# Kernel tuning notes

Hardware: AMD Instinct MI355X
Metric: run time of the kernel (lower is better)

Reference implementation:

```python
import jax, jax.numpy as jnp
import numpy as np

B, T, N, D = 4, 128, 512, 32
CHEB_K, EMB, HEADS, TA_LAYERS, GCN_NUM, TCN_BLOCKS, KSIZE = 3, 10, 2, 2, 3, 3, 3


def setup_inputs() -> dict:
    key = jax.random.key(0)
    ks = jax.random.split(key, 12)
    x = jax.random.normal(ks[0], (B, T, N, D), jnp.float32)
    init_state = jnp.zeros((1, B, N, D), jnp.float32)  # unused by forward, kept for signature fidelity
    node_embeddings = jax.random.normal(ks[1], (N, EMB), jnp.float32)
    a = jax.random.uniform(ks[2], (N, N), jnp.float32)
    a = 0.5 * (a + a.T)
    adj = a / jnp.sum(a, axis=1, keepdims=True)  # row-normalized dense adjacency
    s = 0.05
    gcn_w = jax.random.normal(ks[3], (GCN_NUM, EMB, CHEB_K, D, D), jnp.float32) * s
    gcn_b = jax.random.normal(ks[4], (GCN_NUM, EMB, D), jnp.float32) * s
    tcn_w1 = jax.random.normal(ks[5], (TCN_BLOCKS, D, D, KSIZE), jnp.float32) * s
    tcn_b1 = jnp.zeros((TCN_BLOCKS, D), jnp.float32)
    tcn_w2 = jax.random.normal(ks[6], (TCN_BLOCKS, D, D, KSIZE), jnp.float32) * s
    tcn_b2 = jnp.zeros((TCN_BLOCKS, D), jnp.float32)
    ta_wq = jax.random.normal(ks[7], (TA_LAYERS, D, D), jnp.float32) * s
    ta_wk = jax.random.normal(ks[8], (TA_LAYERS, D, D), jnp.float32) * s
    ta_wv = jax.random.normal(ks[9], (TA_LAYERS, D, D), jnp.float32) * s
    ta_wo = jax.random.normal(ks[10], (TA_LAYERS, D, D), jnp.float32) * s
    ta_g = jnp.ones((TA_LAYERS, D), jnp.float32)
    ta_b = jnp.zeros((TA_LAYERS, D), jnp.float32)
    return dict(x=x, init_state=init_state, node_embeddings=node_embeddings, adj=adj,
                gcn_w=gcn_w, gcn_b=gcn_b, tcn_w1=tcn_w1, tcn_b1=tcn_b1, tcn_w2=tcn_w2,
                tcn_b2=tcn_b2, ta_wq=ta_wq, ta_wk=ta_wk, ta_wv=ta_wv, ta_wo=ta_wo,
                ta_g=ta_g, ta_b=ta_b)


def _cheb_supports(adj, k):
    I = jnp.eye(adj.shape[0], dtype=adj.dtype)
    s = [I, adj]
    for _ in range(2, k):
        s.append(2.0 * (adj @ s[-1]) - s[-2])
    return jnp.stack(s[:k])  # (k, N, N)


def _emb_gcn(h, supports, E, wp, bp):
    # h: (B,T,N,C); supports: (k,N,N); E: (N,EMB); wp: (EMB,k,C,O); bp: (EMB,O)
    xg = jnp.einsum('knm,btmc->btknc', supports, h)
    W = jnp.einsum('ne,ekco->nkco', E, wp)       # per-node Chebyshev weights
    bias = E @ bp                                 # (N,O)
    return jnp.einsum('btknc,nkco->btno', xg, W) + bias


def _causal_conv(y, w, b, dil):
    # y: (BN, C, T); w: (O, C, K)
    pad = (w.shape[-1] - 1) * dil
    out = jax.lax.conv_general_dilated(y, w, (1,), [(pad, 0)], rhs_dilation=(dil,),
                                       dimension_numbers=('NCH', 'OIH', 'NCH'))
    return out + b[None, :, None]


def _temporal_block(y, w1, b1, w2, b2, dil):
    o = jax.nn.relu(_causal_conv(y, w1, b1, dil))
    o = jax.nn.relu(_causal_conv(o, w2, b2, dil))
    return jax.nn.relu(o + y)  # residual (in_ch == out_ch)


def _layernorm(h, g, b):
    mu = jnp.mean(h, -1, keepdims=True)
    var = jnp.var(h, -1, keepdims=True)
    return (h - mu) * jax.lax.rsqrt(var + 1e-5) * g + b


def _attn_layer(h, wq, wk, wv, wo, g, b):
    # h: (BN, T, D) temporal self-attention
    bn, t, d = h.shape
    dh = d // HEADS
    scale = 1.0 / float(np.sqrt(dh))
    q = (h @ wq).reshape(bn, t, HEADS, dh)
    k = (h @ wk).reshape(bn, t, HEADS, dh)
    v = (h @ wv).reshape(bn, t, HEADS, dh)
    a = jax.nn.softmax(jnp.einsum('bqhd,bkhd->bhqk', q, k) * scale, axis=-1)
    o = jnp.einsum('bhqk,bkhd->bqhd', a, v).reshape(bn, t, d) @ wo
    return _layernorm(h + o, g, b)


def reference(x, init_state, node_embeddings, adj, gcn_w, gcn_b, tcn_w1, tcn_b1,
              tcn_w2, tcn_b2, ta_wq, ta_wk, ta_wv, ta_wo, ta_g, ta_b):
    supports = _cheb_supports(adj, CHEB_K)
    h = x
    for i in range(GCN_NUM):  # 3 stacked EmbGCN layers, vectorized over time
        h = _emb_gcn(h, supports, node_embeddings, gcn_w[i], gcn_b[i])
    b, t, n, d = h.shape
    y = jnp.transpose(h, (0, 2, 3, 1)).reshape(b * n, d, t)  # (BN, D, T)
    for i in range(TCN_BLOCKS):  # dilations 1,2,4
        y = _temporal_block(y, tcn_w1[i], tcn_b1[i], tcn_w2[i], tcn_b2[i], 2 ** i)
    h2 = jnp.transpose(y.reshape(b, n, d, t), (0, 1, 3, 2)).reshape(b * n, t, d)
    for i in range(TA_LAYERS):
        h2 = _attn_layer(h2, ta_wq[i], ta_wk[i], ta_wv[i], ta_wo[i], ta_g[i], ta_b[i])
    return jnp.transpose(h2.reshape(b, n, t, d), (0, 2, 1, 3))  # (B,T,N,D)
```

## Files before the change

### kernel.cpp

```cpp
#include <hip/hip_runtime.h>
#include <hip/hip_bf16.h>


typedef __attribute__((ext_vector_type(8))) short short8;
typedef __attribute__((ext_vector_type(4))) short short4v;
typedef __attribute__((ext_vector_type(4))) float float4v;

#define MFMA32(a, b, c) __builtin_amdgcn_mfma_f32_16x16x32_bf16((a), (b), (c), 0, 0, 0)
#if defined(__has_builtin)
#if __has_builtin(__builtin_amdgcn_mfma_f32_16x16x16_bf16)
#define MFMA16A(a, b, c) __builtin_amdgcn_mfma_f32_16x16x16_bf16((a), (b), (c), 0, 0, 0)
#endif
#endif
#ifndef MFMA16A
#define MFMA16A(a, b, c) __builtin_amdgcn_mfma_f32_16x16x16bf16_1k((a), (b), (c), 0, 0, 0)
#endif

#if defined(__has_builtin)
#if __has_builtin(__builtin_amdgcn_exp2f)
#define EXP2F(x) __builtin_amdgcn_exp2f(x)
#endif
#endif
#ifndef EXP2F
#define EXP2F(x) exp2f(x)
#endif

typedef const __attribute__((address_space(1))) unsigned int* gas_ptr;
typedef __attribute__((address_space(3))) unsigned int* las_ptr;
__device__ __forceinline__ void glds16(const void* g, void* l) {
  __builtin_amdgcn_global_load_lds((gas_ptr)g, (las_ptr)l, 16, 0, 0);
}

__device__ __forceinline__ unsigned int f2b2(float lo, float hi) {
  union { __hip_bfloat162 h; unsigned int u; } cv;
  cv.h = __float22bfloat162_rn(make_float2(lo, hi));
  return cv.u;
}
__device__ __forceinline__ unsigned short f2b(float f) {
  return (unsigned short)f2b2(f, f);
}
__device__ __forceinline__ float b2f(unsigned short u) {
  return __uint_as_float(((unsigned int)u) << 16);
}
__device__ __forceinline__ ushort4 f2b4(float a, float b, float c, float d) {
  union { unsigned int u[2]; ushort4 s; } cv;
  cv.u[0] = f2b2(a, b);
  cv.u[1] = f2b2(c, d);
  return cv.s;
}

__global__ void __launch_bounds__(256) prep_all(
    const float* __restrict__ adj, unsigned short* __restrict__ Sb,
    const float* __restrict__ emb, const float* __restrict__ gw,
    const float* __restrict__ gb, unsigned short* __restrict__ W8,
    float* __restrict__ biasn,
    const float* __restrict__ w1g, const float* __restrict__ w2g,
    unsigned short* __restrict__ Wt,
    const float* __restrict__ wqg, const float* __restrict__ wkg,
    const float* __restrict__ wvg, const float* __restrict__ wog,
    unsigned short* __restrict__ Wf,
    const float* __restrict__ x, unsigned short* __restrict__ H8,
    unsigned short* __restrict__ Hrm) {
  __shared__ unsigned short Asq[128 * 40];
  __shared__ unsigned short Bsq[128 * 40];
  int bid = blockIdx.x, tid = threadIdx.x;

  if (bid < 64) {
    int base = bid * 4096;
#pragma unroll
    for (int it = 0; it < 4; ++it) {
      int e = base + it * 1024 + tid * 4;
      float4 v = *(const float4*)&adj[e];
      union { unsigned int u[2]; ushort4 s; } pk;
      pk.u[0] = f2b2(v.x, v.y);
      pk.u[1] = f2b2(v.z, v.w);
      *(ushort4*)&Sb[e] = pk.s;
    }
    return;
  }
  if (bid < 80) {
    int tb = bid - 64;
    int mt = tb >> 2, jt = tb & 3;
    int m0 = mt * 128, j0 = jt * 128;
    int wave = tid >> 6, lane = tid & 63;
    int wm = wave >> 1, wj = wave & 1;
    int l15 = lane & 15, quad = lane >> 4;
    float4v acc[4][4];
#pragma unroll
    for (int a = 0; a < 4; ++a)
#pragma unroll
      for (int b = 0; b < 4; ++b) acc[a][b] = (float4v)0.f;
    for (int kt = 0; kt < 512; kt += 32) {
#pragma unroll
      for (int p = 0; p < 16; ++p) {
        int idx = p * 256 + tid;
        int m = idx >> 5, k = idx & 31;
        Asq[m * 40 + k] = f2b(adj[(m0 + m) * 512 + kt + k]);
      }
#pragma unroll
      for (int p = 0; p < 16; ++p) {
        int idx = p * 256 + tid;
        int k = idx >> 7, j = idx & 127;
        Bsq[j * 40 + k] = f2b(adj[(kt + k) * 512 + j0 + j]);
      }
      __syncthreads();
      short8 af[4], bfr[4];
#pragma unroll
      for (int mi = 0; mi < 4; ++mi)
        af[mi] = *(const short8*)&Asq[(wm * 64 + mi * 16 + l15) * 40 + quad * 8];
#pragma unroll
      for (int ji = 0; ji < 4; ++ji)
        bfr[ji] = *(const short8*)&Bsq[(wj * 64 + ji * 16 + l15) * 40 + quad * 8];
#pragma unroll
      for (int mi = 0; mi < 4; ++mi)
#pragma unroll
        for (int ji = 0; ji < 4; ++ji)
          acc[mi][ji] = MFMA32(af[mi], bfr[ji], acc[mi][ji]);
      __syncthreads();
    }
#pragma unroll
    for (int mi = 0; mi < 4; ++mi)
#pragma unroll
      for (int ji = 0; ji < 4; ++ji) {
        int j = j0 + wj * 64 + ji * 16 + l15;
#pragma unroll
        for (int r = 0; r < 4; ++r) {
          int m = m0 + wm * 64 + mi * 16 + quad * 4 + r;
          Sb[(512 + m) * 512 + j] =
              f2b(2.f * acc[mi][ji][r] - (m == j ? 1.f : 0.f));
        }
      }
    return;
  }
  if (bid < 1616) {
    int b2 = bid - 80;
    int i = b2 >> 9, n = b2 & 511;
    float ev[10];
#pragma unroll
    for (int e = 0; e < 10; ++e) ev[e] = emb[n * 10 + e];
    for (int idx = tid; idx < 3072; idx += 256) {
      int s = idx >> 10, c = (idx >> 5) & 31, o = idx & 31;
      float acc = 0.f;
#pragma unroll
      for (int e = 0; e < 10; ++e) acc += ev[e] * gw[(i * 10 + e) * 3072 + idx];
      W8[((i * 512 + n) * 3 + s) * 1024 + (c >> 3) * 256 + o * 8 + (c & 7)] =
          f2b(acc);
    }
    if (tid < 32) {
      float acc = 0.f;
#pragma unroll
      for (int e = 0; e < 10; ++e) acc += ev[e] * gb[(i * 10 + e) * 32 + tid];
      biasn[(i * 512 + n) * 32 + tid] = acc;
    }
    return;
  }
  if (bid < 1622) {
    int b2 = bid - 1616;
    int blk = b2 >> 1, conv = b2 & 1;
    const float* w = (conv ? w2g : w1g) + blk * 3072;
    for (int idx = tid; idx < 3072; idx += 256) {
      int kk = idx >> 10, rem = idx & 1023;
      int o = rem >> 5, c = rem & 31;
      Wt[b2 * 3072 + idx] = f2b(w[o * 96 + c * 3 + kk]);
    }
    return;
  }
  if (bid < 1654) {
    int idx = (bid - 1622) * 256 + tid;
    int L = idx >> 12;
    int mat = (idx >> 10) & 3;
    int nt = (idx >> 9) & 1;
    int lane = (idx >> 3) & 63;
    int j = idx & 7;
    int quad = lane >> 4, l15 = lane & 15;
    const float* base =
        (mat == 0 ? wqg : mat == 1 ? wkg : mat == 2 ? wvg : wog) + L * 1024;
    float v = base[(quad * 8 + j) * 32 + nt * 16 + l15];
    if (mat == 0) v *= 0.36067376022224085f;
    Wf[idx] = f2b(v);
    return;
  }
  {
    int b2 = bid - 1654;
    int nblk = b2 >> 3, part = b2 & 7;
    for (int qq = tid; qq < 2048; qq += 256) {
      int q = part * 2048 + qq;
      int bt = q >> 5, c = q & 31;
      const float* xb = x + bt * 16384 + nblk * 256 + c;
      float f[8];
#pragma unroll
      for (int s = 0; s < 8; ++s) f[s] = xb[s * 32];
      union { unsigned int u[4]; uint4 v; } pk;
      pk.u[0] = f2b2(f[0], f[1]);
      pk.u[1] = f2b2(f[2], f[3]);
      pk.u[2] = f2b2(f[4], f[5]);
      pk.u[3] = f2b2(f[6], f[7]);
      *(uint4*)&H8[nblk * 131072 + q * 8] = pk.v;
    }
    for (int qq = tid; qq < 2048; qq += 256) {
      int q = part * 2048 + qq;
      int s = q >> 11, e0 = (q & 2047) * 8;
      int bt = e0 >> 5, c0 = e0 & 31;
      const float* xb = x + bt * 16384 + (nblk * 8 + s) * 32 + c0;
      float4 v0 = *(const float4*)&xb[0];
      float4 v1 = *(const float4*)&xb[4];
      union { unsigned int u[4]; uint4 v; } pk;
      pk.u[0] = f2b2(v0.x, v0.y);
      pk.u[1] = f2b2(v0.z, v0.w);
      pk.u[2] = f2b2(v1.x, v1.y);
      pk.u[3] = f2b2(v1.z, v1.w);
      *(uint4*)&Hrm[(nblk * 8 + s) * 16384 + e0] = pk.v;
    }
  }
}

__global__ void __launch_bounds__(512) gcn_phaseA(
    const unsigned short* __restrict__ Sb,
    const unsigned short* __restrict__ H8,
    unsigned short* __restrict__ G) {
  __shared__ unsigned short As[2][256 * 32];
  __shared__ unsigned short Bs[2][4096];
  int bid0 = blockIdx.x;
  int nb = (bid0 & 7) * 64 + (bid0 >> 3);
  int mt = nb & 3, jt = nb >> 2;
  int m0 = mt * 256, j0 = jt * 128;
  int tid = threadIdx.x;
  int wave = tid >> 6, lane = tid & 63;
  int wm = wave >> 1, wj = wave & 1;
  int l15 = lane & 15, quad = lane >> 4;
  float4v acc[4][4];
#pragma unroll
  for (int a = 0; a < 4; ++a)
#pragma unroll
    for (int b = 0; b < 4; ++b) acc[a][b] = (float4v)0.f;

  int qa0 = tid, qa1 = tid + 512;
  int ma0 = qa0 >> 2, ca0 = ((qa0 & 3) ^ ((qa0 >> 3) & 3)) * 8;
  int ma1 = qa1 >> 2, ca1 = ((qa1 & 3) ^ ((qa1 >> 3) & 3)) * 8;
  const unsigned short* sb0 = &Sb[(m0 + ma0) * 512 + ca0];
  const unsigned short* sb1 = &Sb[(m0 + ma1) * 512 + ca1];
  const unsigned short* hb0 = &H8[(tid >> 7) * 131072 + (j0 + (tid & 127)) * 8];

#define STAGE_A(buf, it2)                                   \
  {                                                         \
    int ncn = (it2) * 32;                                   \
    glds16(sb0 + ncn, &As[(buf)][qa0 * 8]);                 \
    glds16(sb1 + ncn, &As[(buf)][qa1 * 8]);                 \
    glds16(hb0 + (ncn >> 3) * 131072, &Bs[(buf)][tid * 8]); \
  }

  STAGE_A(0, 0);
  for (int it = 0; it < 16; ++it) {
    int cur = it & 1;
    if (it < 15) {
      STAGE_A(cur ^ 1, it + 1);
      asm volatile("s_waitcnt vmcnt(3)" ::: "memory");
    } else {
      asm volatile("s_waitcnt vmcnt(0)" ::: "memory");
    }
    __builtin_amdgcn_sched_barrier(0);
    __builtin_amdgcn_s_barrier();
    short8 af[4], bfr[4];
#pragma unroll
    for (int mi = 0; mi < 4; ++mi) {
      int row = wm * 64 + mi * 16 + l15;
      int c8 = quad ^ ((row >> 1) & 3);
      af[mi] = *(const short8*)&As[cur][row * 32 + c8 * 8];
    }
#pragma unroll
    for (int ji = 0; ji < 4; ++ji)
      bfr[ji] =
          *(const short8*)&Bs[cur][quad * 1024 + (wj * 64 + ji * 16 + l15) * 8];
#pragma unroll
    for (int mi = 0; mi < 4; ++mi)
#pragma unroll
      for (int ji = 0; ji < 4; ++ji)
        acc[mi][ji] = MFMA32(af[mi], bfr[ji], acc[mi][ji]);
    __builtin_amdgcn_s_barrier();
  }
#undef STAGE_A
#pragma unroll
  for (int mi = 0; mi < 4; ++mi)
#pragma unroll
    for (int ji = 0; ji < 4; ++ji) {
      int j = j0 + wj * 64 + ji * 16 + l15;
#pragma unroll
      for (int r = 0; r < 4; ++r) {
        int m = m0 + wm * 64 + mi * 16 + quad * 4 + r;
        G[m * 16384 + j] = f2b(acc[mi][ji][r]);
      }
    }
}

__global__ void __launch_bounds__(256) gcn_phaseB(
    const unsigned short* __restrict__ Hrm, const unsigned short* __restrict__ G,
    const unsigned short* __restrict__ W8, const float* __restrict__ biasn,
    unsigned short* __restrict__ H8out, unsigned short* __restrict__ Hrmout,
    unsigned short* __restrict__ tcnout) {
  int bid = blockIdx.x;
  int n = bid >> 1, bh = bid & 1;
  int tid = threadIdx.x;
  int lane = tid & 63, wave = tid >> 6, l15 = lane & 15, quad = lane >> 4;
  short8 wb[3][2];
#pragma unroll
  for (int s = 0; s < 3; ++s)
#pragma unroll
    for (int nt = 0; nt < 2; ++nt)
      wb[s][nt] = *(const short8*)&W8[(n * 3 + s) * 1024 + quad * 256 +
                                      (nt * 16 + l15) * 8];
  float b0 = biasn[n * 32 + l15], b1 = biasn[n * 32 + 16 + l15];
  int n8base = (n >> 3) * 131072 + (n & 7);
#pragma unroll
  for (int mi = 0; mi < 4; ++mi) {
    int bt0 = bh * 256 + wave * 64 + mi * 16;
    int btl = bt0 + l15;
    short8 a0 = *(const short8*)&Hrm[n * 16384 + btl * 32 + quad * 8];
    short8 a1 = *(const short8*)&G[n * 16384 + btl * 32 + quad * 8];
    short8 a2 = *(const short8*)&G[(512 + n) * 16384 + btl * 32 + quad * 8];
    float4v acc0 = MFMA32(a0, wb[0][0], (float4v)0.f);
    acc0 = MFMA32(a1, wb[1][0], acc0);
    acc0 = MFMA32(a2, wb[2][0], acc0);
    float4v acc1 = MFMA32(a0, wb[0][1], (float4v)0.f);
    acc1 = MFMA32(a1, wb[1][1], acc1);
    acc1 = MFMA32(a2, wb[2][1], acc1);
#pragma unroll
    for (int r = 0; r < 4; ++r) {
      int bt = bt0 + quad * 4 + r;
      unsigned short v0 = f2b(acc0[r] + b0);
      unsigned short v1 = f2b(acc1[r] + b1);
      if (tcnout) {
        int bb = bt >> 7, t = bt & 127;
        int o0 = l15, o1 = 16 + l15;
        tcnout[n * 16384 + bb * 4096 + (o0 >> 3) * 1024 + t * 8 + (o0 & 7)] = v0;
        tcnout[n * 16384 + bb * 4096 + (o1 >> 3) * 1024 + t * 8 + (o1 & 7)] = v1;
      } else {
        H8out[n8base + (bt * 32 + l15) * 8] = v0;
        H8out[n8base + (bt * 32 + 16 + l15) * 8] = v1;
        Hrmout[n * 16384 + bt * 32 + l15] = v0;
        Hrmout[n * 16384 + bt * 32 + 16 + l15] = v1;
      }
    }
  }
}

__global__ void __launch_bounds__(256) tcn_kernel(
    const unsigned short* __restrict__ Yin, unsigned short* __restrict__ yout,
    const unsigned short* __restrict__ Wt,
    const float* __restrict__ b1g, const float* __restrict__ b2g) {
  __shared__ unsigned short Y8[4][4352];
  __shared__ unsigned short O8[4][4352];
  int tid = threadIdx.x, wave = tid >> 6, lane = tid & 63;
  int l15 = lane & 15, quad = lane >> 4;
  int n = blockIdx.x, b = wave;
  unsigned short* y8 = &Y8[wave][0];
  unsigned short* o8 = &O8[wave][0];
  {
    int cg = lane >> 4, t = (lane >> 1) & 7, half = lane & 1;
    ushort4 z = {0, 0, 0, 0};
    *(ushort4*)&y8[(cg * 136 + t) * 8 + half * 4] = z;
    *(ushort4*)&o8[(cg * 136 + t) * 8 + half * 4] = z;
  }
  const unsigned short* src = Yin + n * 16384 + b * 4096;
#pragma unroll
  for (int p = 0; p < 8; ++p) {
    int e = p * 64 + lane;
    int cg = e >> 7, t = e & 127;
    *(uint4*)&y8[(cg * 136 + t + 8) * 8] = *(const uint4*)&src[e * 8];
  }
  for (int blk = 0; blk < 3; ++blk) {
    int dil = 1 << blk;
    for (int conv = 0; conv < 2; ++conv) {
      const unsigned short* wbase = Wt + ((blk * 2 + conv) * 3) * 1024;
      short8 af[2][3];
#pragma unroll
      for (int mt = 0; mt < 2; ++mt)
#pragma unroll
        for (int kk = 0; kk < 3; ++kk)
          af[mt][kk] = *(const short8*)&wbase[kk * 1024 +
                                              (mt * 16 + l15) * 32 + quad * 8];
      const float* bias = (conv ? b2g : b1g) + blk * 32;
      float4 bs0 = *(const float4*)&bias[quad * 4];
      float4 bs1 = *(const float4*)&bias[16 + quad * 4];
      float bb0[4] = {bs0.x, bs0.y, bs0.z, bs0.w};
      float bb1[4] = {bs1.x, bs1.y, bs1.z, bs1.w};
      const unsigned short* rbuf = conv ? o8 : y8;
#pragma unroll 2
      for (int nt = 0; nt < 8; ++nt) {
        float4v acc0 = (float4v)0.f, acc1 = (float4v)0.f;
#pragma unroll
        for (int kk = 0; kk < 3; ++kk) {
          int tb = nt * 16 + l15 + 8 - (2 - kk) * dil;
          short8 bf = *(const short8*)&rbuf[(quad * 136 + tb) * 8];
          acc0 = MFMA32(af[0][kk], bf, acc0);
          acc1 = MFMA32(af[1][kk], bf, acc1);
        }
        int t8 = nt * 16 + l15 + 8;
        int og0 = (quad >> 1), ci0 = (quad & 1) * 4;
        if (conv == 0) {
          ushort4 w0 = f2b4(fmaxf(acc0[0] + bb0[0], 0.f),
                            fmaxf(acc0[1] + bb0[1], 0.f),
                            fmaxf(acc0[2] + bb0[2], 0.f),
                            fmaxf(acc0[3] + bb0[3], 0.f));
          ushort4 w1 = f2b4(fmaxf(acc1[0] + bb1[0], 0.f),
                            fmaxf(acc1[1] + bb1[1], 0.f),
                            fmaxf(acc1[2] + bb1[2], 0.f),
                            fmaxf(acc1[3] + bb1[3], 0.f));
          *(ushort4*)&o8[((og0)*136 + t8) * 8 + ci0] = w0;
          *(ushort4*)&o8[((2 + og0) * 136 + t8) * 8 + ci0] = w1;
        } else {
          ushort4 y0 = *(const ushort4*)&y8[((og0)*136 + t8) * 8 + ci0];
          ushort4 y1 = *(const ushort4*)&y8[((2 + og0) * 136 + t8) * 8 + ci0];
          ushort4 w0 = f2b4(
              fmaxf(fmaxf(acc0[0] + bb0[0], 0.f) + b2f(y0.x), 0.f),
              fmaxf(fmaxf(acc0[1] + bb0[1], 0.f) + b2f(y0.y), 0.f),
              fmaxf(fmaxf(acc0[2] + bb0[2], 0.f) + b2f(y0.z), 0.f),
              fmaxf(fmaxf(acc0[3] + bb0[3], 0.f) + b2f(y0.w), 0.f));
          ushort4 w1 = f2b4(
              fmaxf(fmaxf(acc1[0] + bb1[0], 0.f) + b2f(y1.x), 0.f),
              fmaxf(fmaxf(acc1[1] + bb1[1], 0.f) + b2f(y1.y), 0.f),
              fmaxf(fmaxf(acc1[2] + bb1[2], 0.f) + b2f(y1.z), 0.f),
              fmaxf(fmaxf(acc1[3] + bb1[3], 0.f) + b2f(y1.w), 0.f));
          *(ushort4*)&y8[((og0)*136 + t8) * 8 + ci0] = w0;
          *(ushort4*)&y8[((2 + og0) * 136 + t8) * 8 + ci0] = w1;
        }
      }
    }
  }
  unsigned short* dst = yout + n * 16384 + b * 4096;
#pragma unroll
  for (int p = 0; p < 8; ++p) {
    int e = p * 64 + lane;
    int og = e >> 7, t = e & 127;
    *(uint4*)&dst[t * 32 + og * 8] = *(const uint4*)&y8[(og * 136 + t + 8) * 8];
  }
}

__global__ void __launch_bounds__(512) attn_kernel(
    const unsigned short* __restrict__ yin,
    float* __restrict__ outp,
    const unsigned short* __restrict__ Wf,
    const float* __restrict__ gg, const float* __restrict__ bgb) {
  __shared__ unsigned short hfrag[4096];
  __shared__ unsigned short KbOb[5120];
  __shared__ unsigned short QT[32 * 136];
  __shared__ unsigned short VT[32 * 136];
  int bn = blockIdx.x, tid = threadIdx.x;
  int b = bn >> 9, n = bn & 511;
  int lane = tid & 63, wave = tid >> 6;
  int l15 = lane & 15, quad = lane >> 4;
  int mtq = wave;

  {
    int q = tid;
    int t = ((q >> 6) << 4) | (q & 15);
    int cb = (q >> 4) & 3;
    glds16(&yin[n * 16384 + b * 4096 + (t * 4 + cb) * 8], &hfrag[q * 8]);
  }

  for (int L = 0; L < 2; ++L) {
    short8 wf[4][2];
#pragma unroll
    for (int mat = 0; mat < 4; ++mat)
#pragma unroll
      for (int nt = 0; nt < 2; ++nt)
        wf[mat][nt] =
            *(const short8*)&Wf[(((L * 4 + mat) * 2 + nt) * 64 + lane) * 8];
    __syncthreads();
    {
      short8 af = *(const short8*)&hfrag[(mtq * 4 + quad) * 128 + l15 * 8];
      int tbase = mtq * 16 + quad * 4;
#pragma unroll
      for (int nt = 0; nt < 2; ++nt) {
        float4v qa = MFMA32(af, wf[0][nt], (float4v)0.f);
        float4v ka = MFMA32(af, wf[1][nt], (float4v)0.f);
        float4v va = MFMA32(af, wf[2][nt], (float4v)0.f);
        int d = nt * 16 + l15;
#pragma unroll
        for (int r = 0; r < 4; ++r) KbOb[(tbase + r) * 36 + d] = f2b(ka[r]);
        *(ushort4*)&QT[d * 136 + tbase] = f2b4(qa[0], qa[1], qa[2], qa[3]);
        *(ushort4*)&VT[d * 136 + tbase] = f2b4(va[0], va[1], va[2], va[3]);
      }
    }
    __syncthreads();
    float4v oaccT[2];
#pragma unroll
    for (int hh = 0; hh < 2; ++hh) oaccT[hh] = (float4v)0.f;
    for (int hh = 0; hh < 2; ++hh) {
      short4v qb;
#pragma unroll
      for (int jj = 0; jj < 4; ++jj)
        qb[jj] = (short)QT[(hh * 16 + quad * 4 + jj) * 136 + mtq * 16 + l15];
      float4v sacc[8];
#pragma unroll
      for (int st = 0; st < 8; ++st) {
        short4v ka = *(const short4v*)&KbOb[(st * 16 + l15) * 36 + hh * 16 +
                                            quad * 4];
        sacc[st] = MFMA16A(ka, qb, (float4v)0.f);
      }
      float tmx[8];
#pragma unroll
      for (int st = 0; st < 8; ++st)
        tmx[st] = fmaxf(fmaxf(sacc[st][0], sacc[st][1]),
                        fmaxf(sacc[st][2], sacc[st][3]));
      float mx = fmaxf(fmaxf(fmaxf(tmx[0], tmx[1]), fmaxf(tmx[2], tmx[3])),
                       fmaxf(fmaxf(tmx[4], tmx[5]), fmaxf(tmx[6], tmx[7])));
      mx = fmaxf(mx, __shfl_xor(mx, 16));
      mx = fmaxf(mx, __shfl_xor(mx, 32));
      float ps[8];
#pragma unroll
      for (int st = 0; st < 8; ++st) {
#pragma unroll
        for (int r = 0; r < 4; ++r) sacc[st][r] = EXP2F(sacc[st][r] - mx);
        ps[st] = (sacc[st][0] + sacc[st][1]) + (sacc[st][2] + sacc[st][3]);
      }
      float sum = ((ps[0] + ps[1]) + (ps[2] + ps[3])) +
                  ((ps[4] + ps[5]) + (ps[6] + ps[7]));
      sum += __shfl_xor(sum, 16);
      sum += __shfl_xor(sum, 32);
      float inv = 1.f / sum;
#pragma unroll
      for (int st = 0; st < 8; ++st) {
        union { unsigned int u[2]; short4v s; } pv;
        pv.u[0] = f2b2(sacc[st][0], sacc[st][1]);
        pv.u[1] = f2b2(sacc[st][2], sacc[st][3]);
        short4v va = *(const short4v*)&VT[(hh * 16 + l15) * 136 + st * 16 +
                                          quad * 4];
        oaccT[hh] = MFMA16A(va, pv.s, oaccT[hh]);
      }
#pragma unroll
      for (int r = 0; r < 4; ++r) oaccT[hh][r] *= inv;
    }
    __syncthreads();
#pragma unroll
    for (int hh = 0; hh < 2; ++hh)
      *(ushort4*)&KbOb[(mtq * 16 + l15) * 40 + hh * 16 + quad * 4] =
          f2b4(oaccT[hh][0], oaccT[hh][1], oaccT[hh][2], oaccT[hh][3]);
    float gam0 = gg[L * 32 + l15], bet0 = bgb[L * 32 + l15];
    float gam1 = gg[L * 32 + 16 + l15], bet1 = bgb[L * 32 + 16 + l15];
    {
      short8 ofa = *(const short8*)&KbOb[(mtq * 16 + l15) * 40 + quad * 8];
      float4v racc0 = MFMA32(ofa, wf[3][0], (float4v)0.f);
      float4v racc1 = MFMA32(ofa, wf[3][1], (float4v)0.f);
      int hi0 = (mtq * 4 + (l15 >> 3)) * 128 + (l15 & 7);
      int hi1 = (mtq * 4 + 2 + (l15 >> 3)) * 128 + (l15 & 7);
#pragma unroll
      for (int r = 0; r < 4; ++r) {
        int t = mtq * 16 + quad * 4 + r;
        int ro = (quad * 4 + r) * 8;
        float v0 = racc0[r] + b2f(hfrag[hi0 + ro]);
        float v1 = racc1[r] + b2f(hfrag[hi1 + ro]);
        float s = v0 + v1;
        for (int m = 1; m < 16; m <<= 1) s += __shfl_xor(s, m);
        float mu = s * 0.03125f;
        float d0 = v0 - mu, d1 = v1 - mu;
        float q = d0 * d0 + d1 * d1;
        for (int m = 1; m < 16; m <<= 1) q += __shfl_xor(q, m);
        float rs = rsqrtf(q * 0.03125f + 1e-5f);
        float y0 = d0 * rs * gam0 + bet0;
        float y1 = d1 * rs * gam1 + bet1;
        if (L == 0) {
          hfrag[hi0 + ro] = f2b(y0);
          hfrag[hi1 + ro] = f2b(y1);
        } else {
          outp[((b * 128 + t) * 512 + n) * 32 + l15] = y0;
          outp[((b * 128 + t) * 512 + n) * 32 + 16 + l15] = y1;
        }
      }
    }
  }
}

extern "C" void kernel_launch(void* const* d_in, const int* in_sizes, int n_in,
                              void* d_out, int out_size, void* d_ws, size_t ws_size,
                              hipStream_t stream) {
  const float* x    = (const float*)d_in[0];
  const float* emb  = (const float*)d_in[2];
  const float* adj  = (const float*)d_in[3];
  const float* gw   = (const float*)d_in[4];
  const float* gb   = (const float*)d_in[5];
  const float* tw1  = (const float*)d_in[6];
  const float* tb1  = (const float*)d_in[7];
  const float* tw2  = (const float*)d_in[8];
  const float* tb2  = (const float*)d_in[9];
  const float* wq   = (const float*)d_in[10];
  const float* wk   = (const float*)d_in[11];
  const float* wv   = (const float*)d_in[12];
  const float* wo   = (const float*)d_in[13];
  const float* tg   = (const float*)d_in[14];
  const float* tbb  = (const float*)d_in[15];
  float* outp = (float*)d_out;

  char* p = (char*)d_ws;
  unsigned short* Sb  = (unsigned short*)p; p += 1048576;
  unsigned short* W8  = (unsigned short*)p; p += 9437184;
  float* biasn        = (float*)p;          p += 196608;
  unsigned short* G   = (unsigned short*)p; p += 33554432;
  unsigned short* H8a = (unsigned short*)p; p += 16777216;
  unsigned short* H8b = (unsigned short*)p; p += 16777216;
  unsigned short* Hra = (unsigned short*)p; p += 16777216;
  unsigned short* Hrb = (unsigned short*)p; p += 16777216;
  unsigned short* Wt  = (unsigned short*)p; p += 36864;
  unsigned short* Wf  = (unsigned short*)p; p += 16384;

  prep_all<<<dim3(2166), dim3(256), 0, stream>>>(
      adj, Sb, emb, gw, gb, W8, biasn, tw1, tw2, Wt, wq, wk, wv, wo, Wf,
      x, H8a, Hra);

  gcn_phaseA<<<dim3(512), dim3(512), 0, stream>>>(Sb, H8a, G);
  gcn_phaseB<<<dim3(1024), dim3(256), 0, stream>>>(
      Hra, G, W8, biasn, H8b, Hrb, (unsigned short*)nullptr);
  gcn_phaseA<<<dim3(512), dim3(512), 0, stream>>>(Sb, H8b, G);
  gcn_phaseB<<<dim3(1024), dim3(256), 0, stream>>>(
      Hrb, G, W8 + 1572864, biasn + 16384, H8a, Hra, (unsigned short*)nullptr);
  gcn_phaseA<<<dim3(512), dim3(512), 0, stream>>>(Sb, H8a, G);
  gcn_phaseB<<<dim3(1024), dim3(256), 0, stream>>>(
      Hra, G, W8 + 3145728, biasn + 32768, (unsigned short*)nullptr,
      (unsigned short*)nullptr, H8b);

  tcn_kernel<<<dim3(512), dim3(256), 0, stream>>>(H8b, H8a, Wt, tb1, tb2);
  attn_kernel<<<dim3(2048), dim3(512), 0, stream>>>(H8a, outp, Wf, tg, tbb);
}
```

Before: 347.2 us.

## Fuse final GCN phase B with TCN and stage row-major stores via LDS

The last GCN phase-B kernel is merged with the temporal convolution kernel, so GCN outputs go straight into shared memory as TCN input instead of making a round trip through global memory, and one launch is removed. Each block now handles two batches, with two waves per batch splitting the time tiles. That split needs a block-wide barrier after every convolution. The regular phase-B kernel also stages its row-major output in LDS so it can be written out with coalesced 16-byte stores instead of scattered 2-byte stores. The costs are extra synchronisation and fewer waves working on each TCN problem.

Measured after the change: 339.3 us. 1.02x faster.

```diff
diff --git a/kernel.cpp b/kernel.cpp
--- a/kernel.cpp
+++ b/kernel.cpp
@@ -295,8 +295,8 @@
 __global__ void __launch_bounds__(256) gcn_phaseB(
     const unsigned short* __restrict__ Hrm, const unsigned short* __restrict__ G,
     const unsigned short* __restrict__ W8, const float* __restrict__ biasn,
-    unsigned short* __restrict__ H8out, unsigned short* __restrict__ Hrmout,
-    unsigned short* __restrict__ tcnout) {
+    unsigned short* __restrict__ H8out, unsigned short* __restrict__ Hrmout) {
+  __shared__ unsigned short stage[8192];
   int bid = blockIdx.x;
   int n = bid >> 1, bh = bid & 1;
   int tid = threadIdx.x;
@@ -312,7 +312,8 @@
   int n8base = (n >> 3) * 131072 + (n & 7);
 #pragma unroll
   for (int mi = 0; mi < 4; ++mi) {
-    int bt0 = bh * 256 + wave * 64 + mi * 16;
+    int btl0 = wave * 64 + mi * 16;
+    int bt0 = bh * 256 + btl0;
     int btl = bt0 + l15;
     short8 a0 = *(const short8*)&Hrm[n * 16384 + btl * 32 + quad * 8];
     short8 a1 = *(const short8*)&G[n * 16384 + btl * 32 + quad * 8];
@@ -326,47 +327,77 @@
 #pragma unroll
     for (int r = 0; r < 4; ++r) {
       int bt = bt0 + quad * 4 + r;
+      int bl = btl0 + quad * 4 + r;
       unsigned short v0 = f2b(acc0[r] + b0);
       unsigned short v1 = f2b(acc1[r] + b1);
-      if (tcnout) {
-        int bb = bt >> 7, t = bt & 127;
-        int o0 = l15, o1 = 16 + l15;
-        tcnout[n * 16384 + bb * 4096 + (o0 >> 3) * 1024 + t * 8 + (o0 & 7)] = v0;
-        tcnout[n * 16384 + bb * 4096 + (o1 >> 3) * 1024 + t * 8 + (o1 & 7)] = v1;
-      } else {
-        H8out[n8base + (bt * 32 + l15) * 8] = v0;
-        H8out[n8base + (bt * 32 + 16 + l15) * 8] = v1;
-        Hrmout[n * 16384 + bt * 32 + l15] = v0;
-        Hrmout[n * 16384 + bt * 32 + 16 + l15] = v1;
-      }
-    }
-  }
-}
-
-__global__ void __launch_bounds__(256) tcn_kernel(
-    const unsigned short* __restrict__ Yin, unsigned short* __restrict__ yout,
+      H8out[n8base + (bt * 32 + l15) * 8] = v0;
+      H8out[n8base + (bt * 32 + 16 + l15) * 8] = v1;
+      stage[bl * 32 + l15] = v0;
+      stage[bl * 32 + 16 + l15] = v1;
+    }
+  }
+  __syncthreads();
+  unsigned short* dst = Hrmout + n * 16384 + bh * 8192;
+#pragma unroll
+  for (int it = 0; it < 4; ++it) {
+    int i16 = it * 256 + tid;
+    *(uint4*)&dst[i16 * 8] = *(const uint4*)&stage[i16 * 8];
+  }
+}
+
+__global__ void __launch_bounds__(256) gcn_phaseB_tcn(
+    const unsigned short* __restrict__ Hrm, const unsigned short* __restrict__ G,
+    const unsigned short* __restrict__ W8, const float* __restrict__ biasn,
     const unsigned short* __restrict__ Wt,
-    const float* __restrict__ b1g, const float* __restrict__ b2g) {
-  __shared__ unsigned short Y8[4][4352];
-  __shared__ unsigned short O8[4][4352];
-  int tid = threadIdx.x, wave = tid >> 6, lane = tid & 63;
-  int l15 = lane & 15, quad = lane >> 4;
-  int n = blockIdx.x, b = wave;
-  unsigned short* y8 = &Y8[wave][0];
-  unsigned short* o8 = &O8[wave][0];
+    const float* __restrict__ b1g, const float* __restrict__ b2g,
+    unsigned short* __restrict__ yout) {
+  __shared__ unsigned short Y8f[2][4352];
+  __shared__ unsigned short O8f[2][4352];
+  int bid = blockIdx.x;
+  int n = bid >> 1, bh = bid & 1;
+  int tid = threadIdx.x;
+  int lane = tid & 63, wave = tid >> 6, l15 = lane & 15, quad = lane >> 4;
+  int b_local = wave >> 1, half = wave & 1;
   {
-    int cg = lane >> 4, t = (lane >> 1) & 7, half = lane & 1;
+    int cg = lane >> 4, t = (lane >> 1) & 7, hf = lane & 1;
     ushort4 z = {0, 0, 0, 0};
-    *(ushort4*)&y8[(cg * 136 + t) * 8 + half * 4] = z;
-    *(ushort4*)&o8[(cg * 136 + t) * 8 + half * 4] = z;
-  }
-  const unsigned short* src = Yin + n * 16384 + b * 4096;
-#pragma unroll
-  for (int p = 0; p < 8; ++p) {
-    int e = p * 64 + lane;
-    int cg = e >> 7, t = e & 127;
-    *(uint4*)&y8[(cg * 136 + t + 8) * 8] = *(const uint4*)&src[e * 8];
-  }
+    *(ushort4*)&Y8f[b_local][(cg * 136 + t) * 8 + hf * 4] = z;
+    *(ushort4*)&O8f[b_local][(cg * 136 + t) * 8 + hf * 4] = z;
+  }
+  short8 wb[3][2];
+#pragma unroll
+  for (int s = 0; s < 3; ++s)
+#pragma unroll
+    for (int nt = 0; nt < 2; ++nt)
+      wb[s][nt] = *(const short8*)&W8[(n * 3 + s) * 1024 + quad * 256 +
+                                      (nt * 16 + l15) * 8];
+  float b0 = biasn[n * 32 + l15], b1 = biasn[n * 32 + 16 + l15];
+#pragma unroll
+  for (int mi = 0; mi < 4; ++mi) {
+    int btl0 = wave * 64 + mi * 16;
+    int btl = bh * 256 + btl0 + l15;
+    short8 a0 = *(const short8*)&Hrm[n * 16384 + btl * 32 + quad * 8];
+    short8 a1 = *(const short8*)&G[n * 16384 + btl * 32 + quad * 8];
+    short8 a2 = *(const short8*)&G[(512 + n) * 16384 + btl * 32 + quad * 8];
+    float4v acc0 = MFMA32(a0, wb[0][0], (float4v)0.f);
+    acc0 = MFMA32(a1, wb[1][0], acc0);
+    acc0 = MFMA32(a2, wb[2][0], acc0);
+    float4v acc1 = MFMA32(a0, wb[0][1], (float4v)0.f);
+    acc1 = MFMA32(a1, wb[1][1], acc1);
+    acc1 = MFMA32(a2, wb[2][1], acc1);
+#pragma unroll
+    for (int r = 0; r < 4; ++r) {
+      int bl = btl0 + quad * 4 + r;
+      int blb = bl >> 7, t = bl & 127;
+      unsigned short v0 = f2b(acc0[r] + b0);
+      unsigned short v1 = f2b(acc1[r] + b1);
+      Y8f[blb][(((l15 >> 3)) * 136 + t + 8) * 8 + (l15 & 7)] = v0;
+      Y8f[blb][((2 + (l15 >> 3)) * 136 + t + 8) * 8 + (l15 & 7)] = v1;
+    }
+  }
+  __syncthreads();
+  unsigned short* y8 = &Y8f[b_local][0];
+  unsigned short* o8 = &O8f[b_local][0];
   for (int blk = 0; blk < 3; ++blk) {
     int dil = 1 << blk;
     for (int conv = 0; conv < 2; ++conv) {
@@ -384,8 +415,9 @@
       float bb0[4] = {bs0.x, bs0.y, bs0.z, bs0.w};
       float bb1[4] = {bs1.x, bs1.y, bs1.z, bs1.w};
       const unsigned short* rbuf = conv ? o8 : y8;
-#pragma unroll 2
-      for (int nt = 0; nt < 8; ++nt) {
+#pragma unroll
+      for (int ntq = 0; ntq < 4; ++ntq) {
+        int nt = half * 4 + ntq;
         float4v acc0 = (float4v)0.f, acc1 = (float4v)0.f;
 #pragma unroll
         for (int kk = 0; kk < 3; ++kk) {
@@ -424,12 +456,13 @@
           *(ushort4*)&y8[((2 + og0) * 136 + t8) * 8 + ci0] = w1;
         }
       }
-    }
-  }
-  unsigned short* dst = yout + n * 16384 + b * 4096;
-#pragma unroll
-  for (int p = 0; p < 8; ++p) {
-    int e = p * 64 + lane;
+      __syncthreads();
+    }
+  }
+  unsigned short* dst = yout + n * 16384 + (bh * 2 + b_local) * 4096;
+#pragma unroll
+  for (int pp = 0; pp < 4; ++pp) {
+    int e = (half * 4 + pp) * 64 + lane;
     int og = e >> 7, t = e & 127;
     *(uint4*)&dst[t * 32 + og * 8] = *(const uint4*)&y8[(og * 136 + t + 8) * 8];
   }
@@ -608,15 +641,13 @@
 
   gcn_phaseA<<<dim3(512), dim3(512), 0, stream>>>(Sb, H8a, G);
   gcn_phaseB<<<dim3(1024), dim3(256), 0, stream>>>(
-      Hra, G, W8, biasn, H8b, Hrb, (unsigned short*)nullptr);
+      Hra, G, W8, biasn, H8b, Hrb);
   gcn_phaseA<<<dim3(512), dim3(512), 0, stream>>>(Sb, H8b, G);
   gcn_phaseB<<<dim3(1024), dim3(256), 0, stream>>>(
-      Hrb, G, W8 + 1572864, biasn + 16384, H8a, Hra, (unsigned short*)nullptr);
+      Hrb, G, W8 + 1572864, biasn + 16384, H8a, Hra);
   gcn_phaseA<<<dim3(512), dim3(512), 0, stream>>>(Sb, H8a, G);
-  gcn_phaseB<<<dim3(1024), dim3(256), 0, stream>>>(
-      Hra, G, W8 + 3145728, biasn + 32768, (unsigned short*)nullptr,
-      (unsigned short*)nullptr, H8b);
-
-  tcn_kernel<<<dim3(512), dim3(256), 0, stream>>>(H8b, H8a, Wt, tb1, tb2);
-  attn_kernel<<<dim3(2048), dim3(512), 0, stream>>>(H8a, outp, Wf, tg, tbb);
-}
+  gcn_phaseB_tcn<<<dim3(1024), dim3(256), 0, stream>>>(
+      Hra, G, W8 + 3145728, biasn + 32768, Wt, tb1, tb2, H8b);
+
+  attn_kernel<<<dim3(2048), dim3(512), 0, stream>>>(H8b, outp, Wf, tg, tbb);
+}
```
